# Optimization experiments

Hardware: AMD Instinct MI355X
Metric: run time of the kernel (lower is better)

## Reference

```python
import jax, jax.numpy as jnp
import numpy as np

KERNEL_SIZE = 11  # matches init kwarg
EPS = 1e-5       # denominator guard used by the CUDA kernel


def setup_inputs() -> dict:
    key = jax.random.key(0)
    k1, k2 = jax.random.split(key)
    B, C, H, W = 4, 3, 512, 512
    image = jax.random.uniform(k1, (B, C, H, W), dtype=jnp.float32)
    # per-pixel Gaussian sigma map in (0.3, 3.3)
    psf = jax.random.uniform(k2, (B, H, W), dtype=jnp.float32) * 3.0 + 0.3
    return {"image": image, "psf": psf}


def _gauss_psf(image, psf, kernel_size):
    # image: [B,C,H,W]; psf: [B,C,H,W] per-pixel sigma.
    # Gather form: out[p] = sum_q img[q] * k(q) / sum_q k(q),
    # k(q) = exp(-(dx^2+dy^2) / (2*sigma[q]^2 + eps)), q in KxK window,
    # out-of-image neighbors skipped (validity mask).
    r = kernel_size // 2
    H, W = image.shape[-2], image.shape[-1]
    pad = ((0, 0), (0, 0), (r, r), (r, r))
    img_p = jnp.pad(image, pad)
    w_p = jnp.pad(psf, pad)
    m_p = jnp.pad(jnp.ones_like(psf), pad)  # validity mask
    out = jnp.zeros_like(image)
    wsum = jnp.zeros_like(image)
    for dy in range(kernel_size):      # loop over fixed kernel offsets, not data dims
        for dx in range(kernel_size):
            d2 = float((dy - r) ** 2 + (dx - r) ** 2)
            iv = img_p[..., dy:dy + H, dx:dx + W]
            wv = w_p[..., dy:dy + H, dx:dx + W]
            mv = m_p[..., dy:dy + H, dx:dx + W]
            k = mv * jnp.exp(-d2 / (2.0 * wv * wv + EPS))
            out = out + iv * k
            wsum = wsum + k
    return out / wsum  # center tap contributes k=1, so wsum >= 1


def reference(image, psf):
    # psf.unsqueeze(1).expand_as(image): broadcast sigma map over channels
    psf_bc = jnp.broadcast_to(psf[:, None, :, :], image.shape)
    return _gauss_psf(image, psf_bc, KERNEL_SIZE)
```

## Files before the change

### kernel.cpp

```cpp
#include <hip/hip_runtime.h>

#define HH 512
#define WW 512
#define HW (HH * WW)
#define RR 5
#define KS 11
#define EPS_F 1e-5f
#define NLOG2E 1.44269504088896340736f
#define OPW 54
#define NG 10

typedef float f2 __attribute__((ext_vector_type(2)));
__device__ __forceinline__ f2 fma2(f2 a, f2 b, f2 c) { return __builtin_elementwise_fma(a, b, c); }

__global__ __launch_bounds__(256, 6) void gauss_psf_kernel(const float* __restrict__ image,
                                                           const float* __restrict__ psf,
                                                           float* __restrict__ out) {
    __shared__ float4 smH[4][6][64];

    const int lane = threadIdx.x;
    const int ty   = threadIdx.y;
    const int g    = blockIdx.x;
    const int y    = blockIdx.y * 4 + ty;
    const int b    = blockIdx.z;

    const int c0   = (g == NG - 1) ? (WW - OPW) : g * OPW;
    const int col  = c0 - RR + lane;
    const int colc = col < 0 ? 0 : (col > WW - 1 ? WW - 1 : col);
    const float xm = ((unsigned)col < (unsigned)WW) ? 1.0f : 0.0f;

    const float* pw   = psf + (size_t)b * HW;
    const float* img0 = image + (size_t)b * 3 * HW;

    f2 a0p[3], a1p[3], a2p[3], awp[3];
#pragma unroll
    for (int p = 0; p < 3; ++p) {
        a0p[p] = (f2)0.0f; a1p[p] = (f2)0.0f; a2p[p] = (f2)0.0f; awp[p] = (f2)0.0f;
    }

    auto tap = [&](int r, float t, float i0, float i1, float i2) {
        const float t2 = t * t, t4 = t2 * t2, t8 = t4 * t4;
        const float t9 = t8 * t, t16 = t8 * t8, t25 = t16 * t9;

        const int ii = (r - RR) * (r - RR);
        const float u = ii == 0 ? 1.0f : ii == 1 ? t : ii == 4 ? t4
                      : ii == 9 ? t9 : ii == 16 ? t16 : t25;

        const f2 u2  = {u, u};
        const f2 f01 = u2 * (f2){1.0f, t};
        const f2 f23 = u2 * (f2){t4, t9};
        const f2 f45 = u2 * (f2){t16, t25};

        const f2 i0v = {i0, i0}, i1v = {i1, i1}, i2v = {i2, i2};
        a0p[0] = fma2(i0v, f01, a0p[0]);
        a0p[1] = fma2(i0v, f23, a0p[1]);
        a0p[2] = fma2(i0v, f45, a0p[2]);
        a1p[0] = fma2(i1v, f01, a1p[0]);
        a1p[1] = fma2(i1v, f23, a1p[1]);
        a1p[2] = fma2(i1v, f45, a1p[2]);
        a2p[0] = fma2(i2v, f01, a2p[0]);
        a2p[1] = fma2(i2v, f23, a2p[1]);
        a2p[2] = fma2(i2v, f45, a2p[2]);
        awp[0] += f01;
        awp[1] += f23;
        awp[2] += f45;
    };

    if (blockIdx.y >= 2 && blockIdx.y <= 125) {
        const float* pb = img0 + (size_t)(y - RR) * WW + colc;
        const float* wb = pw + (size_t)(y - RR) * WW + colc;
#pragma unroll
        for (int r = 0; r < KS; ++r) {
            const float w  = wb[r * WW];
            const float i0 = pb[r * WW];
            const float i1 = pb[r * WW + HW];
            const float i2 = pb[r * WW + 2 * HW];
            const float a = -NLOG2E * __builtin_amdgcn_rcpf(fmaf(2.0f * w, w, EPS_F));
            const float t = xm * __builtin_amdgcn_exp2f(a);
            tap(r, t, i0, i1, i2);
        }
    } else {
#pragma unroll
        for (int r = 0; r < KS; ++r) {
            const int gy = y - RR + r;
            const int ry = gy < 0 ? 0 : (gy > HH - 1 ? HH - 1 : gy);
            const float ym = ((unsigned)gy < (unsigned)HH) ? 1.0f : 0.0f;
            const int ni = ry * WW + colc;
            const float w  = pw[ni];
            const float i0 = img0[ni];
            const float i1 = img0[ni + HW];
            const float i2 = img0[ni + 2 * HW];
            const float a = -NLOG2E * __builtin_amdgcn_rcpf(fmaf(2.0f * w, w, EPS_F));
            const float t = xm * ym * __builtin_amdgcn_exp2f(a);
            tap(r, t, i0, i1, i2);
        }
    }

#pragma unroll
    for (int p = 0; p < 3; ++p) {
        smH[ty][2 * p][lane]     = make_float4(a0p[p].x, a1p[p].x, a2p[p].x, awp[p].x);
        smH[ty][2 * p + 1][lane] = make_float4(a0p[p].y, a1p[p].y, a2p[p].y, awp[p].y);
    }

    const int lm = lane - RR;
    const int lb = lm < 0 ? 0 : (lm > OPW - 1 ? OPW - 1 : lm);
    f2 s01 = (f2)0.0f, s2w = (f2)0.0f;
#pragma unroll
    for (int j = 0; j < KS; ++j) {
        const int jj = (j - RR) * (j - RR);
        const int ai = jj == 0 ? 0 : jj == 1 ? 1 : jj == 4 ? 2
                     : jj == 9 ? 3 : jj == 16 ? 4 : 5;
        const float4 v = smH[ty][ai][lb + j];
        s01 += (f2){v.x, v.y};
        s2w += (f2){v.z, v.w};
    }

    if ((unsigned)lm < OPW) {
        const float swv = s2w.y;
        float inv = __builtin_amdgcn_rcpf(swv);
        inv = inv * (2.0f - swv * inv);
        const int oi = y * WW + col;
        float* outb = out + (size_t)b * 3 * HW;
        outb[oi]          = s01.x * inv;
        outb[HW + oi]     = s01.y * inv;
        outb[2 * HW + oi] = s2w.x * inv;
    }
}

extern "C" void kernel_launch(void* const* d_in, const int* in_sizes, int n_in,
                              void* d_out, int out_size, void* d_ws, size_t ws_size,
                              hipStream_t stream) {
    const float* image = (const float*)d_in[0];
    const float* psf   = (const float*)d_in[1];
    float* out = (float*)d_out;

    dim3 block(64, 4, 1);
    dim3 grid(NG, HH / 4, 4);
    gauss_psf_kernel<<<grid, block, 0, stream>>>(image, psf, out);
}
```

Measured before the change: 83.33 us.

## Compute two output rows per thread to reuse vertical tap loads and exp

Each thread now produces two vertically adjacent output rows. It loads 12 rows and computes the exp/rcp per row once, then feeds both accumulator sets, which cuts redundant global loads and transcendental work roughly in half. The fast interior path now also drops column clamping and the x-mask for interior column groups. The cost is doubled accumulator registers: launch bounds are lowered from 6 to 4 waves, and the grid is halved in y. Shared memory is reused across two sequential horizontal passes with no barrier, which is safe only because each ty works within a single wavefront.

```diff
diff --git a/kernel.cpp b/kernel.cpp
--- a/kernel.cpp
+++ b/kernel.cpp
@@ -9,11 +9,13 @@
 #define NLOG2E 1.44269504088896340736f
 #define OPW 54
 #define NG 10
+#define RPW 2
+#define NR (KS + RPW - 1)
 
 typedef float f2 __attribute__((ext_vector_type(2)));
 __device__ __forceinline__ f2 fma2(f2 a, f2 b, f2 c) { return __builtin_elementwise_fma(a, b, c); }
 
-__global__ __launch_bounds__(256, 6) void gauss_psf_kernel(const float* __restrict__ image,
+__global__ __launch_bounds__(256, 4) void gauss_psf_kernel(const float* __restrict__ image,
                                                            const float* __restrict__ psf,
                                                            float* __restrict__ out) {
     __shared__ float4 smH[4][6][64];
@@ -21,7 +23,8 @@
     const int lane = threadIdx.x;
     const int ty   = threadIdx.y;
     const int g    = blockIdx.x;
-    const int y    = blockIdx.y * 4 + ty;
+    const int by   = blockIdx.y;
+    const int yA   = by * (4 * RPW) + ty * RPW;
     const int b    = blockIdx.z;
 
     const int c0   = (g == NG - 1) ? (WW - OPW) : g * OPW;
@@ -32,57 +35,69 @@
     const float* pw   = psf + (size_t)b * HW;
     const float* img0 = image + (size_t)b * 3 * HW;
 
-    f2 a0p[3], a1p[3], a2p[3], awp[3];
+    f2 A0[3], A1[3], A2[3], Aw[3], B0[3], B1[3], B2[3], Bw[3];
 #pragma unroll
     for (int p = 0; p < 3; ++p) {
-        a0p[p] = (f2)0.0f; a1p[p] = (f2)0.0f; a2p[p] = (f2)0.0f; awp[p] = (f2)0.0f;
+        A0[p] = (f2)0.0f; A1[p] = (f2)0.0f; A2[p] = (f2)0.0f; Aw[p] = (f2)0.0f;
+        B0[p] = (f2)0.0f; B1[p] = (f2)0.0f; B2[p] = (f2)0.0f; Bw[p] = (f2)0.0f;
     }
 
-    auto tap = [&](int r, float t, float i0, float i1, float i2) {
-        const float t2 = t * t, t4 = t2 * t2, t8 = t4 * t4;
-        const float t9 = t8 * t, t16 = t8 * t8, t25 = t16 * t9;
-
-        const int ii = (r - RR) * (r - RR);
-        const float u = ii == 0 ? 1.0f : ii == 1 ? t : ii == 4 ? t4
-                      : ii == 9 ? t9 : ii == 16 ? t16 : t25;
-
+    auto accum = [&](f2 (&a0)[3], f2 (&a1)[3], f2 (&a2)[3], f2 (&aw)[3],
+                     float u, float t, float t4, float t9, float t16, float t25,
+                     float i0, float i1, float i2) {
         const f2 u2  = {u, u};
         const f2 f01 = u2 * (f2){1.0f, t};
         const f2 f23 = u2 * (f2){t4, t9};
         const f2 f45 = u2 * (f2){t16, t25};
-
         const f2 i0v = {i0, i0}, i1v = {i1, i1}, i2v = {i2, i2};
-        a0p[0] = fma2(i0v, f01, a0p[0]);
-        a0p[1] = fma2(i0v, f23, a0p[1]);
-        a0p[2] = fma2(i0v, f45, a0p[2]);
-        a1p[0] = fma2(i1v, f01, a1p[0]);
-        a1p[1] = fma2(i1v, f23, a1p[1]);
-        a1p[2] = fma2(i1v, f45, a1p[2]);
-        a2p[0] = fma2(i2v, f01, a2p[0]);
-        a2p[1] = fma2(i2v, f23, a2p[1]);
-        a2p[2] = fma2(i2v, f45, a2p[2]);
-        awp[0] += f01;
-        awp[1] += f23;
-        awp[2] += f45;
+        a0[0] = fma2(i0v, f01, a0[0]);
+        a0[1] = fma2(i0v, f23, a0[1]);
+        a0[2] = fma2(i0v, f45, a0[2]);
+        a1[0] = fma2(i1v, f01, a1[0]);
+        a1[1] = fma2(i1v, f23, a1[1]);
+        a1[2] = fma2(i1v, f45, a1[2]);
+        a2[0] = fma2(i2v, f01, a2[0]);
+        a2[1] = fma2(i2v, f23, a2[1]);
+        a2[2] = fma2(i2v, f45, a2[2]);
+        aw[0] += f01;
+        aw[1] += f23;
+        aw[2] += f45;
     };
 
-    if (blockIdx.y >= 2 && blockIdx.y <= 125) {
-        const float* pb = img0 + (size_t)(y - RR) * WW + colc;
-        const float* wb = pw + (size_t)(y - RR) * WW + colc;
+    auto row = [&](int r, float t, float i0, float i1, float i2) {
+        const float t2 = t * t, t4 = t2 * t2, t8 = t4 * t4;
+        const float t9 = t8 * t, t16 = t8 * t8, t25 = t16 * t9;
+        if (r <= KS - 1) {
+            const int ii = (r - RR) * (r - RR);
+            const float u = ii == 0 ? 1.0f : ii == 1 ? t : ii == 4 ? t4
+                          : ii == 9 ? t9 : ii == 16 ? t16 : t25;
+            accum(A0, A1, A2, Aw, u, t, t4, t9, t16, t25, i0, i1, i2);
+        }
+        if (r >= 1) {
+            const int ii = (r - 1 - RR) * (r - 1 - RR);
+            const float u = ii == 0 ? 1.0f : ii == 1 ? t : ii == 4 ? t4
+                          : ii == 9 ? t9 : ii == 16 ? t16 : t25;
+            accum(B0, B1, B2, Bw, u, t, t4, t9, t16, t25, i0, i1, i2);
+        }
+    };
+
+    if (g >= 1 && g <= 8 && by >= 1 && by <= 62) {
+        const float* pb = img0 + (size_t)(yA - RR) * WW + col;
+        const float* wb = pw + (size_t)(yA - RR) * WW + col;
 #pragma unroll
-        for (int r = 0; r < KS; ++r) {
+        for (int r = 0; r < NR; ++r) {
             const float w  = wb[r * WW];
             const float i0 = pb[r * WW];
             const float i1 = pb[r * WW + HW];
             const float i2 = pb[r * WW + 2 * HW];
             const float a = -NLOG2E * __builtin_amdgcn_rcpf(fmaf(2.0f * w, w, EPS_F));
-            const float t = xm * __builtin_amdgcn_exp2f(a);
-            tap(r, t, i0, i1, i2);
+            const float t = __builtin_amdgcn_exp2f(a);
+            row(r, t, i0, i1, i2);
         }
     } else {
 #pragma unroll
-        for (int r = 0; r < KS; ++r) {
-            const int gy = y - RR + r;
+        for (int r = 0; r < NR; ++r) {
+            const int gy = yA - RR + r;
             const int ry = gy < 0 ? 0 : (gy > HH - 1 ? HH - 1 : gy);
             const float ym = ((unsigned)gy < (unsigned)HH) ? 1.0f : 0.0f;
             const int ni = ry * WW + colc;
@@ -92,39 +107,43 @@
             const float i2 = img0[ni + 2 * HW];
             const float a = -NLOG2E * __builtin_amdgcn_rcpf(fmaf(2.0f * w, w, EPS_F));
             const float t = xm * ym * __builtin_amdgcn_exp2f(a);
-            tap(r, t, i0, i1, i2);
+            row(r, t, i0, i1, i2);
         }
-    }
-
-#pragma unroll
-    for (int p = 0; p < 3; ++p) {
-        smH[ty][2 * p][lane]     = make_float4(a0p[p].x, a1p[p].x, a2p[p].x, awp[p].x);
-        smH[ty][2 * p + 1][lane] = make_float4(a0p[p].y, a1p[p].y, a2p[p].y, awp[p].y);
     }
 
     const int lm = lane - RR;
     const int lb = lm < 0 ? 0 : (lm > OPW - 1 ? OPW - 1 : lm);
-    f2 s01 = (f2)0.0f, s2w = (f2)0.0f;
+    float* outb = out + (size_t)b * 3 * HW;
+
+    auto passH = [&](f2 (&a0)[3], f2 (&a1)[3], f2 (&a2)[3], f2 (&aw)[3], int y) {
 #pragma unroll
-    for (int j = 0; j < KS; ++j) {
-        const int jj = (j - RR) * (j - RR);
-        const int ai = jj == 0 ? 0 : jj == 1 ? 1 : jj == 4 ? 2
-                     : jj == 9 ? 3 : jj == 16 ? 4 : 5;
-        const float4 v = smH[ty][ai][lb + j];
-        s01 += (f2){v.x, v.y};
-        s2w += (f2){v.z, v.w};
-    }
+        for (int p = 0; p < 3; ++p) {
+            smH[ty][2 * p][lane]     = make_float4(a0[p].x, a1[p].x, a2[p].x, aw[p].x);
+            smH[ty][2 * p + 1][lane] = make_float4(a0[p].y, a1[p].y, a2[p].y, aw[p].y);
+        }
+        f2 s01 = (f2)0.0f, s2w = (f2)0.0f;
+#pragma unroll
+        for (int j = 0; j < KS; ++j) {
+            const int jj = (j - RR) * (j - RR);
+            const int ai = jj == 0 ? 0 : jj == 1 ? 1 : jj == 4 ? 2
+                         : jj == 9 ? 3 : jj == 16 ? 4 : 5;
+            const float4 v = smH[ty][ai][lb + j];
+            s01 += (f2){v.x, v.y};
+            s2w += (f2){v.z, v.w};
+        }
+        if ((unsigned)lm < OPW) {
+            const float swv = s2w.y;
+            float inv = __builtin_amdgcn_rcpf(swv);
+            inv = inv * (2.0f - swv * inv);
+            const int oi = y * WW + col;
+            outb[oi]          = s01.x * inv;
+            outb[HW + oi]     = s01.y * inv;
+            outb[2 * HW + oi] = s2w.x * inv;
+        }
+    };
 
-    if ((unsigned)lm < OPW) {
-        const float swv = s2w.y;
-        float inv = __builtin_amdgcn_rcpf(swv);
-        inv = inv * (2.0f - swv * inv);
-        const int oi = y * WW + col;
-        float* outb = out + (size_t)b * 3 * HW;
-        outb[oi]          = s01.x * inv;
-        outb[HW + oi]     = s01.y * inv;
-        outb[2 * HW + oi] = s2w.x * inv;
-    }
+    passH(A0, A1, A2, Aw, yA);
+    passH(B0, B1, B2, Bw, yA + 1);
 }
 
 extern "C" void kernel_launch(void* const* d_in, const int* in_sizes, int n_in,
@@ -135,6 +154,6 @@
     float* out = (float*)d_out;
 
     dim3 block(64, 4, 1);
-    dim3 grid(NG, HH / 4, 4);
+    dim3 grid(NG, HH / (4 * RPW), 4);
     gauss_psf_kernel<<<grid, block, 0, stream>>>(image, psf, out);
 }
```

Result: faster. 81.67 us (median of 2 runs) (-2.0%).
